# Kernel tuning notes

Hardware: AMD Instinct MI355X
Metric: run time of the kernel (lower is better)

Reference implementation:

```python
import jax, jax.numpy as jnp
import numpy as np

N, F, A = 8192, 64, 16
H1, H2 = 128, 64  # hidden_dims
E = 16 * N


def _dense_params(key, din, dout):
    kw, kb = jax.random.split(key)
    W = jax.random.normal(kw, (din, dout), dtype=jnp.float32) * (1.0 / np.sqrt(din))
    b = jnp.zeros((dout,), dtype=jnp.float32)
    return W, b


def setup_inputs() -> dict:
    key = jax.random.key(0)
    ks = jax.random.split(key, 12)
    nodes = jax.random.normal(ks[0], (N, F), dtype=jnp.float32)
    edges = jax.random.randint(ks[1], (E, 2), 0, N, dtype=jnp.int32)
    adjacency = jax.random.uniform(ks[2], (N, N), dtype=jnp.float32) * (2.0 / N)
    actions = jax.random.normal(ks[3], (N, A), dtype=jnp.float32)
    We1, be1 = _dense_params(ks[4], F, H1)
    We2, be2 = _dense_params(ks[5], H1, H2)
    Weo, beo = _dense_params(ks[6], H2, H2)   # encoder output Dense -> output_dim = hidden_dims[-1]
    Wc1, bc1 = _dense_params(ks[7], H2 + A, H1)
    Wc2, bc2 = _dense_params(ks[8], H1, H2)
    Wq, bq = _dense_params(ks[9], H2, 1)
    return {"nodes": nodes, "edges": edges, "adjacency": adjacency, "actions": actions,
            "We1": We1, "be1": be1, "We2": We2, "be2": be2, "Weo": Weo, "beo": beo,
            "Wc1": Wc1, "bc1": bc1, "Wc2": Wc2, "bc2": bc2, "Wq": Wq, "bq": bq}


def reference(nodes, edges, adjacency, actions,
              We1, be1, We2, be2, Weo, beo,
              Wc1, bc1, Wc2, bc2, Wq, bq):
    # GraphEncoder: per hidden layer Dense -> relu -> adjacency aggregation, then output Dense
    x = jax.nn.relu(nodes @ We1 + be1)      # [N, H1]
    x = adjacency @ x                        # message passing (memory-bound)
    x = jax.nn.relu(x @ We2 + be2)          # [N, H2]
    x = adjacency @ x
    emb = x @ Weo + beo                      # [N, H2]
    # Critic head: concat actions, MLP, scalar Q per node
    h = jnp.concatenate([emb, actions], axis=-1)  # [N, H2+A]
    h = jax.nn.relu(h @ Wc1 + bc1)
    h = jax.nn.relu(h @ Wc2 + bc2)
    q = h @ Wq + bq                          # [N, 1]
    return q.squeeze(-1)
```

## Files before the change

### kernel.cpp

```cpp
#include <hip/hip_runtime.h>

typedef __bf16 bf16;
typedef __bf16 bf16x8 __attribute__((ext_vector_type(8)));
typedef float f32x4 __attribute__((ext_vector_type(4)));

#define NN 8192

__device__ inline bf16x8 cvt8(float4 lo, float4 hi) {
  bf16x8 r;
  r[0] = (__bf16)lo.x; r[1] = (__bf16)lo.y; r[2] = (__bf16)lo.z; r[3] = (__bf16)lo.w;
  r[4] = (__bf16)hi.x; r[5] = (__bf16)hi.y; r[6] = (__bf16)hi.z; r[7] = (__bf16)hi.w;
  return r;
}

__global__ __launch_bounds__(256) void k_enc1(const float* __restrict__ nodes,
                                              const float* __restrict__ We1,
                                              const float* __restrict__ be1,
                                              bf16* __restrict__ B1p) {
  __shared__ float Ns[32 * 68];
  __shared__ bf16 Os[128 * 40];
  int tid = threadIdx.x;
  int r0 = blockIdx.x * 32;
  for (int idx = tid; idx < 512; idx += 256) {
    int r = idx >> 4, c4 = (idx & 15) * 4;
    *(float4*)(&Ns[r * 68 + c4]) = *(const float4*)(nodes + (r0 + r) * 64 + c4);
  }
  __syncthreads();
  int c = tid & 127, rb = tid >> 7;
  float acc[16];
  float b = be1[c];
#pragma unroll
  for (int k = 0; k < 16; ++k) acc[k] = b;
  for (int f = 0; f < 64; ++f) {
    float wv = We1[f * 128 + c];
#pragma unroll
    for (int k = 0; k < 16; ++k)
      acc[k] = fmaf(Ns[(rb + 2 * k) * 68 + f], wv, acc[k]);
  }
#pragma unroll
  for (int k = 0; k < 16; ++k) {
    float v = acc[k] > 0.f ? acc[k] : 0.f;
    Os[c * 40 + rb + 2 * k] = (bf16)v;
  }
  __syncthreads();
  int c2 = tid >> 1, h = tid & 1;
  const uint4* src = (const uint4*)(Os + c2 * 40 + h * 16);
  uint4* dst = (uint4*)(B1p + (size_t)(r0 / 32) * 128 * 32 + c2 * 32 + h * 16);
  dst[0] = src[0]; dst[1] = src[1];
}

struct AF { float4 q[4]; };

template <int NCG>
__global__ __launch_bounds__(256, 4) void k_pass(const float* __restrict__ A,
                                                 const bf16* __restrict__ Bp,
                                                 float* __restrict__ Out,
                                                 int KL) {
  constexpr int COLS = 2 * NCG * 16;
  int tid = threadIdx.x;
  int lane = tid & 63, w = tid >> 6;
  int rowg = w >> 1, colg = w & 1;
  int l15 = lane & 15, lg = lane >> 4;
  int klane = lg * 8;
  int r0 = blockIdx.x * 64 + rowg * 32;
  int kbase = blockIdx.y * KL;
  const float* pa0 = A + (size_t)(r0 + l15) * NN + kbase + klane;
  const float* pa1 = pa0 + (size_t)16 * NN;
  const bf16* bbase = Bp + ((size_t)(kbase >> 5) * COLS + colg * (NCG * 16) + l15) * 32 + klane;

  f32x4 acc[2][NCG];
#pragma unroll
  for (int m = 0; m < 2; ++m)
#pragma unroll
    for (int cg = 0; cg < NCG; ++cg) acc[m][cg] = (f32x4){0.f, 0.f, 0.f, 0.f};

  auto LDA = [&](int kt, AF& f) {
    f.q[0] = *(const float4*)(pa0 + kt);
    f.q[1] = *(const float4*)(pa0 + kt + 4);
    f.q[2] = *(const float4*)(pa1 + kt);
    f.q[3] = *(const float4*)(pa1 + kt + 4);
  };
  auto LDB = [&](int kt, uint4* b) {
    const bf16* p = bbase + (size_t)(kt >> 5) * (COLS * 32);
#pragma unroll
    for (int cg = 0; cg < NCG; ++cg) b[cg] = *(const uint4*)(p + cg * 512);
  };
  auto CMP = [&](const AF& f, const uint4* b) {
    bf16x8 a0 = cvt8(f.q[0], f.q[1]);
    bf16x8 a1 = cvt8(f.q[2], f.q[3]);
#pragma unroll
    for (int cg = 0; cg < NCG; ++cg) {
      bf16x8 bfr = __builtin_bit_cast(bf16x8, b[cg]);
      acc[0][cg] = __builtin_amdgcn_mfma_f32_16x16x32_bf16(a0, bfr, acc[0][cg], 0, 0, 0);
      acc[1][cg] = __builtin_amdgcn_mfma_f32_16x16x32_bf16(a1, bfr, acc[1][cg], 0, 0, 0);
    }
  };

  AF a0f, a1f;
  uint4 b0[NCG], b1[NCG];
  LDA(0, a0f);
  LDB(0, b0);
  int ktail = KL - 64;
  int kt = 0;
  for (; kt < ktail; kt += 64) {
    LDA(kt + 32, a1f);
    LDB(kt + 32, b1);
    CMP(a0f, b0);
    LDA(kt + 64, a0f);
    LDB(kt + 64, b0);
    CMP(a1f, b1);
  }
  LDA(kt + 32, a1f);
  LDB(kt + 32, b1);
  CMP(a0f, b0);
  CMP(a1f, b1);

  float* out = Out + (size_t)blockIdx.y * NN * COLS;
#pragma unroll
  for (int m = 0; m < 2; ++m)
#pragma unroll
    for (int cg = 0; cg < NCG; ++cg)
#pragma unroll
      for (int i = 0; i < 4; ++i)
        out[(size_t)(r0 + m * 16 + lg * 4 + i) * COLS + colg * (NCG * 16) + cg * 16 + l15] = acc[m][cg][i];
}

__global__ __launch_bounds__(256) void k_mid(const float* __restrict__ X2p,
                                             const float* __restrict__ We2,
                                             const float* __restrict__ be2,
                                             bf16* __restrict__ B3p, int KS) {
  __shared__ float X2s[32 * 128];
  __shared__ bf16 Os[64 * 40];
  int tid = threadIdx.x;
  int r0 = blockIdx.x * 32;
  for (int idx = tid; idx < 1024; idx += 256) {
    int r = idx >> 5, c4 = (idx & 31) * 4;
    float4 u = {0.f, 0.f, 0.f, 0.f};
    for (int p = 0; p < KS; ++p) {
      float4 v = *(const float4*)(X2p + (size_t)p * NN * 128 + (size_t)(r0 + r) * 128 + c4);
      u.x += v.x; u.y += v.y; u.z += v.z; u.w += v.w;
    }
    *(float4*)(&X2s[r * 128 + c4]) = u;
  }
  __syncthreads();
  int c = tid & 63, rb = tid >> 6;
  float acc[8];
  float b = be2[c];
#pragma unroll
  for (int k = 0; k < 8; ++k) acc[k] = b;
  for (int j = 0; j < 128; ++j) {
    float wv = We2[j * 64 + c];
#pragma unroll
    for (int k = 0; k < 8; ++k)
      acc[k] = fmaf(X2s[(rb + 4 * k) * 128 + j], wv, acc[k]);
  }
#pragma unroll
  for (int k = 0; k < 8; ++k) {
    float v = acc[k] > 0.f ? acc[k] : 0.f;
    Os[c * 40 + rb + 4 * k] = (bf16)v;
  }
  __syncthreads();
  int c2 = tid >> 2, h = tid & 3;
  const uint4* src = (const uint4*)(Os + c2 * 40 + h * 8);
  uint4* dst = (uint4*)(B3p + (size_t)(r0 / 32) * 64 * 32 + c2 * 32 + h * 8);
  dst[0] = src[0];
}

__global__ __launch_bounds__(256) void k_head(const float* __restrict__ X4p,
                                              const float* __restrict__ actions,
                                              const float* __restrict__ Weo,
                                              const float* __restrict__ beo,
                                              const float* __restrict__ Wc1,
                                              const float* __restrict__ bc1,
                                              const float* __restrict__ Wc2,
                                              const float* __restrict__ bc2,
                                              const float* __restrict__ Wq,
                                              const float* __restrict__ bq,
                                              float* __restrict__ q, int KS) {
  __shared__ float X4s[32 * 65];
  __shared__ float hs[32 * 81];
  __shared__ float h1s[32 * 129];
  __shared__ float h2s[32 * 65];
  int tid = threadIdx.x;
  int r0 = blockIdx.x * 32;
  for (int idx = tid; idx < 2048; idx += 256) {
    int r = idx >> 6, c = idx & 63;
    float s = 0.f;
    for (int p = 0; p < KS; ++p)
      s += X4p[(size_t)p * NN * 64 + (size_t)(r0 + r) * 64 + c];
    X4s[r * 65 + c] = s;
  }
  for (int idx = tid; idx < 512; idx += 256) {
    int r = idx >> 4, a = idx & 15;
    hs[r * 81 + 64 + a] = actions[(r0 + r) * 16 + a];
  }
  __syncthreads();
  {
    int c = tid & 63, rb = tid >> 6;
    float acc[8];
    float b = beo[c];
#pragma unroll
    for (int k = 0; k < 8; ++k) acc[k] = b;
    for (int j = 0; j < 64; ++j) {
      float wv = Weo[j * 64 + c];
#pragma unroll
      for (int k = 0; k < 8; ++k)
        acc[k] = fmaf(X4s[(rb + 4 * k) * 65 + j], wv, acc[k]);
    }
#pragma unroll
    for (int k = 0; k < 8; ++k) hs[(rb + 4 * k) * 81 + c] = acc[k];
  }
  __syncthreads();
  {
    int c = tid & 127, rb = tid >> 7;
    float acc[16];
    float b = bc1[c];
#pragma unroll
    for (int k = 0; k < 16; ++k) acc[k] = b;
    for (int j = 0; j < 80; ++j) {
      float wv = Wc1[j * 128 + c];
#pragma unroll
      for (int k = 0; k < 16; ++k)
        acc[k] = fmaf(hs[(rb + 2 * k) * 81 + j], wv, acc[k]);
    }
#pragma unroll
    for (int k = 0; k < 16; ++k) {
      float v = acc[k] > 0.f ? acc[k] : 0.f;
      h1s[(rb + 2 * k) * 129 + c] = v;
    }
  }
  __syncthreads();
  {
    int c = tid & 63, rb = tid >> 6;
    float acc[8];
    float b = bc2[c];
#pragma unroll
    for (int k = 0; k < 8; ++k) acc[k] = b;
    for (int j = 0; j < 128; ++j) {
      float wv = Wc2[j * 64 + c];
#pragma unroll
      for (int k = 0; k < 8; ++k)
        acc[k] = fmaf(h1s[(rb + 4 * k) * 129 + j], wv, acc[k]);
    }
#pragma unroll
    for (int k = 0; k < 8; ++k) {
      float v = acc[k] > 0.f ? acc[k] : 0.f;
      h2s[(rb + 4 * k) * 65 + c] = v;
    }
  }
  __syncthreads();
  if (tid < 32) {
    float acc = bq[0];
    for (int j = 0; j < 64; ++j) acc = fmaf(h2s[tid * 65 + j], Wq[j], acc);
    q[r0 + tid] = acc;
  }
}

extern "C" void kernel_launch(void* const* d_in, const int* in_sizes, int n_in,
                              void* d_out, int out_size, void* d_ws, size_t ws_size,
                              hipStream_t stream) {
  const float* nodes = (const float*)d_in[0];
  const float* A = (const float*)d_in[2];
  const float* actions = (const float*)d_in[3];
  const float* We1 = (const float*)d_in[4];
  const float* be1 = (const float*)d_in[5];
  const float* We2 = (const float*)d_in[6];
  const float* be2 = (const float*)d_in[7];
  const float* Weo = (const float*)d_in[8];
  const float* beo = (const float*)d_in[9];
  const float* Wc1 = (const float*)d_in[10];
  const float* bc1 = (const float*)d_in[11];
  const float* Wc2 = (const float*)d_in[12];
  const float* bc2 = (const float*)d_in[13];
  const float* Wq = (const float*)d_in[14];
  const float* bq = (const float*)d_in[15];
  float* q = (float*)d_out;

  const size_t MB = 1ull << 20;
  int KS = 2;
  if (ws_size >= 3 * MB + 8 * 6 * MB) KS = 8;
  else if (ws_size >= 3 * MB + 4 * 6 * MB) KS = 4;

  char* ws = (char*)d_ws;
  bf16* B1p = (bf16*)(ws);
  bf16* B3p = (bf16*)(ws + 2 * MB);
  float* X2p = (float*)(ws + 3 * MB);
  float* X4p = (float*)(ws + 3 * MB + (size_t)KS * 4 * MB);

  int KL = NN / KS;
  k_enc1<<<256, 256, 0, stream>>>(nodes, We1, be1, B1p);
  k_pass<4><<<dim3(128, KS), 256, 0, stream>>>(A, B1p, X2p, KL);
  k_mid<<<256, 256, 0, stream>>>(X2p, We2, be2, B3p, KS);
  k_pass<2><<<dim3(128, KS), 256, 0, stream>>>(A, B3p, X4p, KL);
  k_head<<<256, 256, 0, stream>>>(X4p, actions, Weo, beo, Wc1, bc1, Wc2, bc2, Wq, bq, q, KS);
}
```

Baseline: 270.9 us.

## Permute K layout for strided A loads, raise split-K to 16, tune occupancy

```diff
diff --git a/kernel.cpp b/kernel.cpp
--- a/kernel.cpp
+++ b/kernel.cpp
@@ -5,6 +5,10 @@
 typedef float f32x4 __attribute__((ext_vector_type(4)));
 
 #define NN 8192
+
+__device__ inline int pinv32(int k) {
+  return ((k >> 2) & 3) * 8 + (k & 3) + ((k & 16) ? 4 : 0);
+}
 
 __device__ inline bf16x8 cvt8(float4 lo, float4 hi) {
   bf16x8 r;
@@ -40,33 +44,33 @@
 #pragma unroll
   for (int k = 0; k < 16; ++k) {
     float v = acc[k] > 0.f ? acc[k] : 0.f;
-    Os[c * 40 + rb + 2 * k] = (bf16)v;
+    Os[c * 40 + pinv32(rb + 2 * k)] = (bf16)v;
   }
   __syncthreads();
   int c2 = tid >> 1, h = tid & 1;
   const uint4* src = (const uint4*)(Os + c2 * 40 + h * 16);
-  uint4* dst = (uint4*)(B1p + (size_t)(r0 / 32) * 128 * 32 + c2 * 32 + h * 16);
+  uint4* dst = (uint4*)(B1p + (size_t)blockIdx.x * 128 * 32 + c2 * 32 + h * 16);
   dst[0] = src[0]; dst[1] = src[1];
 }
 
 struct AF { float4 q[4]; };
 
-template <int NCG>
-__global__ __launch_bounds__(256, 4) void k_pass(const float* __restrict__ A,
-                                                 const bf16* __restrict__ Bp,
-                                                 float* __restrict__ Out,
-                                                 int KL) {
-  constexpr int COLS = 2 * NCG * 16;
+template <int NCG, int MINW>
+__global__ __launch_bounds__(256, MINW) void k_pass(const float* __restrict__ A,
+                                                    const bf16* __restrict__ Bp,
+                                                    float* __restrict__ Out,
+                                                    int KL) {
+  constexpr int COLS = 32 * NCG;
   int tid = threadIdx.x;
   int lane = tid & 63, w = tid >> 6;
   int rowg = w >> 1, colg = w & 1;
   int l15 = lane & 15, lg = lane >> 4;
-  int klane = lg * 8;
   int r0 = blockIdx.x * 64 + rowg * 32;
-  int kbase = blockIdx.y * KL;
-  const float* pa0 = A + (size_t)(r0 + l15) * NN + kbase + klane;
+  int c0 = colg * (NCG * 16);
+  int kbase = blockIdx.z * KL;
+  const float* pa0 = A + (size_t)(r0 + l15) * NN + kbase + lg * 4;
   const float* pa1 = pa0 + (size_t)16 * NN;
-  const bf16* bbase = Bp + ((size_t)(kbase >> 5) * COLS + colg * (NCG * 16) + l15) * 32 + klane;
+  const bf16* bbase = Bp + ((size_t)(kbase >> 5) * COLS + c0 + l15) * 32 + lg * 8;
 
   f32x4 acc[2][NCG];
 #pragma unroll
@@ -76,9 +80,9 @@
 
   auto LDA = [&](int kt, AF& f) {
     f.q[0] = *(const float4*)(pa0 + kt);
-    f.q[1] = *(const float4*)(pa0 + kt + 4);
+    f.q[1] = *(const float4*)(pa0 + kt + 16);
     f.q[2] = *(const float4*)(pa1 + kt);
-    f.q[3] = *(const float4*)(pa1 + kt + 4);
+    f.q[3] = *(const float4*)(pa1 + kt + 16);
   };
   auto LDB = [&](int kt, uint4* b) {
     const bf16* p = bbase + (size_t)(kt >> 5) * (COLS * 32);
@@ -115,14 +119,14 @@
   CMP(a0f, b0);
   CMP(a1f, b1);
 
-  float* out = Out + (size_t)blockIdx.y * NN * COLS;
+  float* out = Out + (size_t)blockIdx.z * NN * COLS;
 #pragma unroll
   for (int m = 0; m < 2; ++m)
 #pragma unroll
     for (int cg = 0; cg < NCG; ++cg)
 #pragma unroll
       for (int i = 0; i < 4; ++i)
-        out[(size_t)(r0 + m * 16 + lg * 4 + i) * COLS + colg * (NCG * 16) + cg * 16 + l15] = acc[m][cg][i];
+        out[(size_t)(r0 + m * 16 + lg * 4 + i) * COLS + c0 + cg * 16 + l15] = acc[m][cg][i];
 }
 
 __global__ __launch_bounds__(256) void k_mid(const float* __restrict__ X2p,
@@ -157,12 +161,12 @@
 #pragma unroll
   for (int k = 0; k < 8; ++k) {
     float v = acc[k] > 0.f ? acc[k] : 0.f;
-    Os[c * 40 + rb + 4 * k] = (bf16)v;
+    Os[c * 40 + pinv32(rb + 4 * k)] = (bf16)v;
   }
   __syncthreads();
   int c2 = tid >> 2, h = tid & 3;
   const uint4* src = (const uint4*)(Os + c2 * 40 + h * 8);
-  uint4* dst = (uint4*)(B3p + (size_t)(r0 / 32) * 64 * 32 + c2 * 32 + h * 8);
+  uint4* dst = (uint4*)(B3p + (size_t)blockIdx.x * 64 * 32 + c2 * 32 + h * 8);
   dst[0] = src[0];
 }
 
@@ -277,9 +281,10 @@
   float* q = (float*)d_out;
 
   const size_t MB = 1ull << 20;
-  int KS = 2;
-  if (ws_size >= 3 * MB + 8 * 6 * MB) KS = 8;
-  else if (ws_size >= 3 * MB + 4 * 6 * MB) KS = 4;
+  int KS = 16;
+  if (ws_size < 3 * MB + 16 * 6 * MB) KS = 8;
+  if (ws_size < 3 * MB + 8 * 6 * MB) KS = 4;
+  if (ws_size < 3 * MB + 4 * 6 * MB) KS = 2;
 
   char* ws = (char*)d_ws;
   bf16* B1p = (bf16*)(ws);
@@ -289,8 +294,8 @@
 
   int KL = NN / KS;
   k_enc1<<<256, 256, 0, stream>>>(nodes, We1, be1, B1p);
-  k_pass<4><<<dim3(128, KS), 256, 0, stream>>>(A, B1p, X2p, KL);
+  k_pass<4, 4><<<dim3(128, 1, KS), 256, 0, stream>>>(A, B1p, X2p, KL);
   k_mid<<<256, 256, 0, stream>>>(X2p, We2, be2, B3p, KS);
-  k_pass<2><<<dim3(128, KS), 256, 0, stream>>>(A, B3p, X4p, KL);
+  k_pass<2, 5><<<dim3(128, 1, KS), 256, 0, stream>>>(A, B3p, X4p, KL);
   k_head<<<256, 256, 0, stream>>>(X4p, actions, Weo, beo, Wc1, bc1, Wc2, bc2, Wq, bq, q, KS);
 }
```

Measured after the change: 316.5 us. 16.8% more time.

## Stage adjacency tiles through LDS with async global_load_lds double buffering

Applied to the files above, without the earlier changes.

```diff
diff --git a/kernel.cpp b/kernel.cpp
--- a/kernel.cpp
+++ b/kernel.cpp
@@ -11,6 +11,12 @@
   r[0] = (__bf16)lo.x; r[1] = (__bf16)lo.y; r[2] = (__bf16)lo.z; r[3] = (__bf16)lo.w;
   r[4] = (__bf16)hi.x; r[5] = (__bf16)hi.y; r[6] = (__bf16)hi.z; r[7] = (__bf16)hi.w;
   return r;
+}
+
+__device__ inline void gload16(const float* g, float* l) {
+  __builtin_amdgcn_global_load_lds(
+      (const __attribute__((address_space(1))) unsigned int*)g,
+      (__attribute__((address_space(3))) unsigned int*)l, 16, 0, 0);
 }
 
 __global__ __launch_bounds__(256) void k_enc1(const float* __restrict__ nodes,
@@ -45,84 +51,90 @@
   __syncthreads();
   int c2 = tid >> 1, h = tid & 1;
   const uint4* src = (const uint4*)(Os + c2 * 40 + h * 16);
-  uint4* dst = (uint4*)(B1p + (size_t)(r0 / 32) * 128 * 32 + c2 * 32 + h * 16);
+  uint4* dst = (uint4*)(B1p + (size_t)blockIdx.x * 128 * 32 + c2 * 32 + h * 16);
   dst[0] = src[0]; dst[1] = src[1];
 }
 
-struct AF { float4 q[4]; };
-
-template <int NCG>
+template <int NF>
 __global__ __launch_bounds__(256, 4) void k_pass(const float* __restrict__ A,
                                                  const bf16* __restrict__ Bp,
                                                  float* __restrict__ Out,
                                                  int KL) {
-  constexpr int COLS = 2 * NCG * 16;
+  constexpr int COLS = NF * 64;
+  __shared__ float Abuf[2][4096];
   int tid = threadIdx.x;
   int lane = tid & 63, w = tid >> 6;
-  int rowg = w >> 1, colg = w & 1;
   int l15 = lane & 15, lg = lane >> 4;
-  int klane = lg * 8;
-  int r0 = blockIdx.x * 64 + rowg * 32;
+  int r0 = blockIdx.x * 32;
   int kbase = blockIdx.y * KL;
-  const float* pa0 = A + (size_t)(r0 + l15) * NN + kbase + klane;
-  const float* pa1 = pa0 + (size_t)16 * NN;
-  const bf16* bbase = Bp + ((size_t)(kbase >> 5) * COLS + colg * (NCG * 16) + l15) * 32 + klane;
-
-  f32x4 acc[2][NCG];
+
+  const float* pstg[4];
+#pragma unroll
+  for (int j = 0; j < 4; ++j) {
+    int row = j * 8 + (tid >> 5);
+    int c = tid & 31;
+    int col = (((c >> 1) ^ (row & 7)) << 3) + ((c & 1) << 2);
+    pstg[j] = A + (size_t)(r0 + row) * NN + kbase + col;
+  }
+  const bf16* pb[NF];
+#pragma unroll
+  for (int nf = 0; nf < NF; ++nf) {
+    int col = w * (NF * 16) + nf * 16 + l15;
+    pb[nf] = Bp + (size_t)(kbase >> 5) * (COLS * 32) + col * 32 + lg * 8;
+  }
+
+  f32x4 acc[2][NF];
 #pragma unroll
   for (int m = 0; m < 2; ++m)
 #pragma unroll
-    for (int cg = 0; cg < NCG; ++cg) acc[m][cg] = (f32x4){0.f, 0.f, 0.f, 0.f};
-
-  auto LDA = [&](int kt, AF& f) {
-    f.q[0] = *(const float4*)(pa0 + kt);
-    f.q[1] = *(const float4*)(pa0 + kt + 4);
-    f.q[2] = *(const float4*)(pa1 + kt);
-    f.q[3] = *(const float4*)(pa1 + kt + 4);
-  };
-  auto LDB = [&](int kt, uint4* b) {
-    const bf16* p = bbase + (size_t)(kt >> 5) * (COLS * 32);
-#pragma unroll
-    for (int cg = 0; cg < NCG; ++cg) b[cg] = *(const uint4*)(p + cg * 512);
-  };
-  auto CMP = [&](const AF& f, const uint4* b) {
-    bf16x8 a0 = cvt8(f.q[0], f.q[1]);
-    bf16x8 a1 = cvt8(f.q[2], f.q[3]);
-#pragma unroll
-    for (int cg = 0; cg < NCG; ++cg) {
-      bf16x8 bfr = __builtin_bit_cast(bf16x8, b[cg]);
-      acc[0][cg] = __builtin_amdgcn_mfma_f32_16x16x32_bf16(a0, bfr, acc[0][cg], 0, 0, 0);
-      acc[1][cg] = __builtin_amdgcn_mfma_f32_16x16x32_bf16(a1, bfr, acc[1][cg], 0, 0, 0);
-    }
-  };
-
-  AF a0f, a1f;
-  uint4 b0[NCG], b1[NCG];
-  LDA(0, a0f);
-  LDB(0, b0);
-  int ktail = KL - 64;
-  int kt = 0;
-  for (; kt < ktail; kt += 64) {
-    LDA(kt + 32, a1f);
-    LDB(kt + 32, b1);
-    CMP(a0f, b0);
-    LDA(kt + 64, a0f);
-    LDB(kt + 64, b0);
-    CMP(a1f, b1);
-  }
-  LDA(kt + 32, a1f);
-  LDB(kt + 32, b1);
-  CMP(a0f, b0);
-  CMP(a1f, b1);
+    for (int nf = 0; nf < NF; ++nf) acc[m][nf] = (f32x4){0.f, 0.f, 0.f, 0.f};
+
+  int NSTEP = KL >> 7;
+#pragma unroll
+  for (int j = 0; j < 4; ++j)
+    gload16(pstg[j], &Abuf[0][j * 1024 + tid * 4]);
+
+  for (int s = 0; s < NSTEP; ++s) {
+    __syncthreads();
+    int cur = s & 1;
+    uint4 b[4][NF];
+#pragma unroll
+    for (int kf = 0; kf < 4; ++kf)
+#pragma unroll
+      for (int nf = 0; nf < NF; ++nf)
+        b[kf][nf] = *(const uint4*)(pb[nf] + (size_t)(s * 4 + kf) * (COLS * 32));
+    if (s + 1 < NSTEP) {
+#pragma unroll
+      for (int j = 0; j < 4; ++j)
+        gload16(pstg[j] + (s + 1) * 128, &Abuf[cur ^ 1][j * 1024 + tid * 4]);
+    }
+#pragma unroll
+    for (int kf = 0; kf < 4; ++kf) {
+#pragma unroll
+      for (int m = 0; m < 2; ++m) {
+        int row = m * 16 + l15;
+        int sl = (((kf * 4 + lg) ^ (row & 7)) << 3);
+        const float* ap = &Abuf[cur][row * 128 + sl];
+        float4 r1 = *(const float4*)ap;
+        float4 r2 = *(const float4*)(ap + 4);
+        bf16x8 a = cvt8(r1, r2);
+#pragma unroll
+        for (int nf = 0; nf < NF; ++nf)
+          acc[m][nf] = __builtin_amdgcn_mfma_f32_16x16x32_bf16(
+              a, __builtin_bit_cast(bf16x8, b[kf][nf]), acc[m][nf], 0, 0, 0);
+      }
+    }
+  }
 
   float* out = Out + (size_t)blockIdx.y * NN * COLS;
 #pragma unroll
   for (int m = 0; m < 2; ++m)
 #pragma unroll
-    for (int cg = 0; cg < NCG; ++cg)
+    for (int nf = 0; nf < NF; ++nf)
 #pragma unroll
       for (int i = 0; i < 4; ++i)
-        out[(size_t)(r0 + m * 16 + lg * 4 + i) * COLS + colg * (NCG * 16) + cg * 16 + l15] = acc[m][cg][i];
+        out[(size_t)(r0 + m * 16 + lg * 4 + i) * COLS + w * (NF * 16) + nf * 16 + l15] =
+            acc[m][nf][i];
 }
 
 __global__ __launch_bounds__(256) void k_mid(const float* __restrict__ X2p,
@@ -162,7 +174,7 @@
   __syncthreads();
   int c2 = tid >> 2, h = tid & 3;
   const uint4* src = (const uint4*)(Os + c2 * 40 + h * 8);
-  uint4* dst = (uint4*)(B3p + (size_t)(r0 / 32) * 64 * 32 + c2 * 32 + h * 8);
+  uint4* dst = (uint4*)(B3p + (size_t)blockIdx.x * 64 * 32 + c2 * 32 + h * 8);
   dst[0] = src[0];
 }
 
@@ -277,9 +289,8 @@
   float* q = (float*)d_out;
 
   const size_t MB = 1ull << 20;
-  int KS = 2;
-  if (ws_size >= 3 * MB + 8 * 6 * MB) KS = 8;
-  else if (ws_size >= 3 * MB + 4 * 6 * MB) KS = 4;
+  int KS = 4;
+  if (ws_size < 3 * MB + 4 * 6 * MB) KS = 2;
 
   char* ws = (char*)d_ws;
   bf16* B1p = (bf16*)(ws);
@@ -289,8 +300,8 @@
 
   int KL = NN / KS;
   k_enc1<<<256, 256, 0, stream>>>(nodes, We1, be1, B1p);
-  k_pass<4><<<dim3(128, KS), 256, 0, stream>>>(A, B1p, X2p, KL);
+  k_pass<2><<<dim3(256, KS), 256, 0, stream>>>(A, B1p, X2p, KL);
   k_mid<<<256, 256, 0, stream>>>(X2p, We2, be2, B3p, KS);
-  k_pass<2><<<dim3(128, KS), 256, 0, stream>>>(A, B3p, X4p, KL);
+  k_pass<1><<<dim3(256, KS), 256, 0, stream>>>(A, B3p, X4p, KL);
   k_head<<<256, 256, 0, stream>>>(X4p, actions, Weo, beo, Wc1, bc1, Wc2, bc2, Wq, bq, q, KS);
 }
```

After: 276.2 us. About the same (+1.9%).
